# Kernel tuning notes

Hardware: AMD Instinct MI355X
Metric: run time of the kernel (lower is better)

## Reference

```python
import jax, jax.numpy as jnp
import numpy as np

K = 3   # num nearest neighbors (init k)
P = 2   # IDW power (init p)


def setup_inputs() -> dict:
    key = jax.random.key(0)
    k1, k2, k3, k4 = jax.random.split(key, 4)
    B, N, M, C = 8, 16384, 1024, 256
    xyz = jax.random.normal(k1, (B, N, 3), dtype=jnp.float32)
    sampled_xyz = jax.random.normal(k2, (B, M, 3), dtype=jnp.float32)
    sampled_features = jax.random.normal(k3, (B, M, C), dtype=jnp.float32)
    masks = jax.random.randint(k4, (B, N), 0, 2, dtype=jnp.int32)
    return {"xyz": xyz, "sampled_xyz": sampled_xyz,
            "sampled_features": sampled_features, "masks": masks}


def reference(xyz, sampled_xyz, sampled_features, masks):
    # xyz: [B,N,3], sampled_xyz: [B,M,3], sampled_features: [B,M,C], masks: [B,N]
    # Squared pairwise distances [B,N,M] (same math as the chunked torch loop).
    delta = xyz[:, :, None, :] - sampled_xyz[:, None, :, :]
    dists = jnp.sum(delta * delta, axis=-1)
    # k smallest distances -> negate and take top-k.
    neg_top, idx = jax.lax.top_k(-dists, K)          # [B,N,K]
    min_dists = jnp.maximum(-neg_top, 1e-10)
    weights = 1.0 / (min_dists ** P + 1e-10)
    weights = weights / jnp.sum(weights, axis=-1, keepdims=True)
    # Gather neighbor features: [B,N,K,C]
    gathered = jax.vmap(lambda f, i: f[i])(sampled_features, idx)
    interpolated = jnp.sum(gathered * weights[..., None], axis=2)  # [B,N,C]
    # Invalid (masked-out) rows stay zero, matching the padded scatter.
    valid = (masks != 0).astype(interpolated.dtype)
    return interpolated * valid[..., None]
```

## Files before the change

### kernel.cpp

```cpp
#include <hip/hip_runtime.h>

constexpr int B = 8;
constexpr int N = 16384;
constexpr int M = 1024;
constexpr int C = 256;
constexpr int PTS = 128;
constexpr int NW  = 8;
constexpr int CPW = M / NW;

__global__ __launch_bounds__(512, 8) void upsample_idw_kernel(
    const float* __restrict__ xyz,
    const float* __restrict__ sxyz,
    const float* __restrict__ feats,
    const int*   __restrict__ masks,
    float*       __restrict__ out)
{
    const int tid = threadIdx.x;
    const int w   = tid >> 6;
    const int l   = tid & 63;
    const int blk = blockIdx.x;
    const int b     = blk >> 7;
    const int nbase = (blk & 127) << 7;

    __shared__ unsigned long long s_key[PTS][NW][3];
    float4* s_cand = (float4*)&s_key[0][0][0];
    __shared__ float s_w[PTS][3];
    __shared__ int   s_j[PTS][4];

    {
        const float* sp = sxyz + (size_t)b * (M * 3);
        #pragma unroll
        for (int t = tid; t < M; t += 512) {
            const float cx = sp[3 * t + 0];
            const float cy = sp[3 * t + 1];
            const float cz = sp[3 * t + 2];
            s_cand[t] = make_float4(cx, cy, cz, 0.f);
        }
    }

    const float* xpA = xyz + ((size_t)b * N + nbase + l) * 3;
    const float* xpB = xyz + ((size_t)b * N + nbase + l + 64) * 3;
    const float xA = xpA[0], yA = xpA[1], zA = xpA[2];
    const float xB = xpB[0], yB = xpB[1], zB = xpB[2];
    __syncthreads();

    const float4* cp = s_cand + w * CPW;

    float a0 = __builtin_inff(), a1 = __builtin_inff(), a2 = __builtin_inff();
    float b0 = __builtin_inff(), b1 = __builtin_inff(), b2 = __builtin_inff();
    int   ia0 = 0, ia1 = 0, ia2 = 0;
    int   ib0 = 0, ib1 = 0, ib2 = 0;

    #pragma unroll 2
    for (int m = 0; m < CPW; ++m) {
        const float4 c = cp[m];
        {
            const float dx = __fsub_rn(xA, c.x);
            const float dy = __fsub_rn(yA, c.y);
            const float dz = __fsub_rn(zA, c.z);
            const float d  = __fadd_rn(__fadd_rn(__fmul_rn(dx, dx), __fmul_rn(dy, dy)),
                                       __fmul_rn(dz, dz));
            const bool lt0 = d < a0, lt1 = d < a1, lt2 = d < a2;
            ia2 = lt1 ? ia1 : (lt2 ? m : ia2);
            ia1 = lt0 ? ia0 : (lt1 ? m : ia1);
            ia0 = lt0 ? m   : ia0;
            const float nd2 = __builtin_amdgcn_fmed3f(a1, a2, d);
            const float nd1 = __builtin_amdgcn_fmed3f(a0, a1, d);
            a2 = nd2; a1 = nd1; a0 = fminf(a0, d);
        }
        {
            const float dx = __fsub_rn(xB, c.x);
            const float dy = __fsub_rn(yB, c.y);
            const float dz = __fsub_rn(zB, c.z);
            const float d  = __fadd_rn(__fadd_rn(__fmul_rn(dx, dx), __fmul_rn(dy, dy)),
                                       __fmul_rn(dz, dz));
            const bool lt0 = d < b0, lt1 = d < b1, lt2 = d < b2;
            ib2 = lt1 ? ib1 : (lt2 ? m : ib2);
            ib1 = lt0 ? ib0 : (lt1 ? m : ib1);
            ib0 = lt0 ? m   : ib0;
            const float nd2 = __builtin_amdgcn_fmed3f(b1, b2, d);
            const float nd1 = __builtin_amdgcn_fmed3f(b0, b1, d);
            b2 = nd2; b1 = nd1; b0 = fminf(b0, d);
        }
    }
    __syncthreads();

    const unsigned base = (unsigned)(w * CPW);
    s_key[l][w][0]      = ((unsigned long long)__float_as_uint(a0) << 32) | (base + (unsigned)ia0);
    s_key[l][w][1]      = ((unsigned long long)__float_as_uint(a1) << 32) | (base + (unsigned)ia1);
    s_key[l][w][2]      = ((unsigned long long)__float_as_uint(a2) << 32) | (base + (unsigned)ia2);
    s_key[l + 64][w][0] = ((unsigned long long)__float_as_uint(b0) << 32) | (base + (unsigned)ib0);
    s_key[l + 64][w][1] = ((unsigned long long)__float_as_uint(b1) << 32) | (base + (unsigned)ib1);
    s_key[l + 64][w][2] = ((unsigned long long)__float_as_uint(b2) << 32) | (base + (unsigned)ib2);
    __syncthreads();

    if (tid < PTS) {
        unsigned long long k0 = ~0ULL, k1 = ~0ULL, k2 = ~0ULL;
        #pragma unroll
        for (int q = 0; q < NW; ++q) {
            #pragma unroll
            for (int s = 0; s < 3; ++s) {
                const unsigned long long k = s_key[tid][q][s];
                const bool lt0 = k < k0, lt1 = k < k1, lt2 = k < k2;
                k2 = lt1 ? k1 : (lt2 ? k : k2);
                k1 = lt0 ? k0 : (lt1 ? k : k1);
                k0 = lt0 ? k  : k0;
            }
        }
        const float e0 = __uint_as_float((unsigned)(k0 >> 32));
        const float e1 = __uint_as_float((unsigned)(k1 >> 32));
        const float e2 = __uint_as_float((unsigned)(k2 >> 32));
        const float m0 = fmaxf(e0, 1e-10f);
        const float m1 = fmaxf(e1, 1e-10f);
        const float m2 = fmaxf(e2, 1e-10f);
        float w0 = 1.0f / (m0 * m0 + 1e-10f);
        float w1 = 1.0f / (m1 * m1 + 1e-10f);
        float w2 = 1.0f / (m2 * m2 + 1e-10f);
        const int valid = masks[(size_t)b * N + nbase + tid];
        const float scale = valid ? (1.0f / (w0 + w1 + w2)) : 0.0f;
        s_w[tid][0] = w0 * scale;
        s_w[tid][1] = w1 * scale;
        s_w[tid][2] = w2 * scale;
        s_j[tid][0] = (int)(unsigned)k0;
        s_j[tid][1] = (int)(unsigned)k1;
        s_j[tid][2] = (int)(unsigned)k2;
        s_j[tid][3] = valid;
    }
    __syncthreads();

    const int pq = tid >> 6;
    const int cq = tid & 63;
    const float4* Fb4 = (const float4*)(feats + (size_t)b * (M * C));
    float4* op4 = (float4*)(out + (((size_t)b * N + nbase) * C));

    for (int p0 = 0; p0 < PTS; p0 += 8) {
        const int p = p0 + pq;
        const int vld = __builtin_amdgcn_readfirstlane(s_j[p][3]);
        float4 acc = make_float4(0.f, 0.f, 0.f, 0.f);
        if (vld) {
            const int j0 = __builtin_amdgcn_readfirstlane(s_j[p][0]);
            const int j1 = __builtin_amdgcn_readfirstlane(s_j[p][1]);
            const int j2 = __builtin_amdgcn_readfirstlane(s_j[p][2]);
            const float w0 = __uint_as_float(
                __builtin_amdgcn_readfirstlane((int)__float_as_uint(s_w[p][0])));
            const float w1 = __uint_as_float(
                __builtin_amdgcn_readfirstlane((int)__float_as_uint(s_w[p][1])));
            const float w2 = __uint_as_float(
                __builtin_amdgcn_readfirstlane((int)__float_as_uint(s_w[p][2])));
            const float4 f0 = Fb4[j0 * 64 + cq];
            const float4 f1 = Fb4[j1 * 64 + cq];
            const float4 f2 = Fb4[j2 * 64 + cq];
            acc.x = fmaf(w2, f2.x, fmaf(w1, f1.x, w0 * f0.x));
            acc.y = fmaf(w2, f2.y, fmaf(w1, f1.y, w0 * f0.y));
            acc.z = fmaf(w2, f2.z, fmaf(w1, f1.z, w0 * f0.z));
            acc.w = fmaf(w2, f2.w, fmaf(w1, f1.w, w0 * f0.w));
        }
        op4[p * 64 + cq] = acc;
    }
}

extern "C" void kernel_launch(void* const* d_in, const int* in_sizes, int n_in,
                              void* d_out, int out_size, void* d_ws, size_t ws_size,
                              hipStream_t stream) {
    const float* xyz   = (const float*)d_in[0];
    const float* sxyz  = (const float*)d_in[1];
    const float* feats = (const float*)d_in[2];
    const int*   masks = (const int*)d_in[3];
    float*       out   = (float*)d_out;

    dim3 grid(B * N / PTS);
    dim3 block(512);
    hipLaunchKernelGGL(upsample_idw_kernel, grid, block, 0, stream,
                       xyz, sxyz, feats, masks, out);
}
```

Before: 79.93 us.

## Load candidate points via scalar loads into SGPRs instead of LDS staging

Replaces the shared-memory staging of sampled points with inline-asm s_load_dwordx16 scalar loads that bring 16 candidates at a time into SGPRs per wave. This removes the LDS fill, one barrier and the per-iteration LDS reads in the distance loop. The block-to-batch mapping is also interleaved so consecutive blocks hit different batches. The cost is a scalar-memory wait per chunk and reliance on inline asm with the SGPR pressure that brings.

```diff
diff --git a/kernel.cpp b/kernel.cpp
--- a/kernel.cpp
+++ b/kernel.cpp
@@ -6,7 +6,8 @@
 constexpr int C = 256;
 constexpr int PTS = 128;
 constexpr int NW  = 8;
-constexpr int CPW = M / NW;
+
+typedef float vf16 __attribute__((ext_vector_type(16)));
 
 __global__ __launch_bounds__(512, 8) void upsample_idw_kernel(
     const float* __restrict__ xyz,
@@ -19,73 +20,75 @@
     const int w   = tid >> 6;
     const int l   = tid & 63;
     const int blk = blockIdx.x;
-    const int b     = blk >> 7;
-    const int nbase = (blk & 127) << 7;
+    const int b     = blk & 7;
+    const int nbase = (blk >> 3) << 7;
 
     __shared__ unsigned long long s_key[PTS][NW][3];
-    float4* s_cand = (float4*)&s_key[0][0][0];
     __shared__ float s_w[PTS][3];
     __shared__ int   s_j[PTS][4];
 
-    {
-        const float* sp = sxyz + (size_t)b * (M * 3);
-        #pragma unroll
-        for (int t = tid; t < M; t += 512) {
-            const float cx = sp[3 * t + 0];
-            const float cy = sp[3 * t + 1];
-            const float cz = sp[3 * t + 2];
-            s_cand[t] = make_float4(cx, cy, cz, 0.f);
-        }
-    }
-
     const float* xpA = xyz + ((size_t)b * N + nbase + l) * 3;
-    const float* xpB = xyz + ((size_t)b * N + nbase + l + 64) * 3;
+    const float* xpB = xyz + ((size_t)b * N + nbase + 64 + l) * 3;
     const float xA = xpA[0], yA = xpA[1], zA = xpA[2];
     const float xB = xpB[0], yB = xpB[1], zB = xpB[2];
-    __syncthreads();
 
-    const float4* cp = s_cand + w * CPW;
+    const float* bbase = sxyz + (size_t)b * (M * 3);
+    const int qoff = __builtin_amdgcn_readfirstlane((tid >> 6) * (128 * 12));
 
     float a0 = __builtin_inff(), a1 = __builtin_inff(), a2 = __builtin_inff();
     float b0 = __builtin_inff(), b1 = __builtin_inff(), b2 = __builtin_inff();
     int   ia0 = 0, ia1 = 0, ia2 = 0;
     int   ib0 = 0, ib1 = 0, ib2 = 0;
 
-    #pragma unroll 2
-    for (int m = 0; m < CPW; ++m) {
-        const float4 c = cp[m];
-        {
-            const float dx = __fsub_rn(xA, c.x);
-            const float dy = __fsub_rn(yA, c.y);
-            const float dz = __fsub_rn(zA, c.z);
-            const float d  = __fadd_rn(__fadd_rn(__fmul_rn(dx, dx), __fmul_rn(dy, dy)),
-                                       __fmul_rn(dz, dz));
-            const bool lt0 = d < a0, lt1 = d < a1, lt2 = d < a2;
-            ia2 = lt1 ? ia1 : (lt2 ? m : ia2);
-            ia1 = lt0 ? ia0 : (lt1 ? m : ia1);
-            ia0 = lt0 ? m   : ia0;
-            const float nd2 = __builtin_amdgcn_fmed3f(a1, a2, d);
-            const float nd1 = __builtin_amdgcn_fmed3f(a0, a1, d);
-            a2 = nd2; a1 = nd1; a0 = fminf(a0, d);
-        }
-        {
-            const float dx = __fsub_rn(xB, c.x);
-            const float dy = __fsub_rn(yB, c.y);
-            const float dz = __fsub_rn(zB, c.z);
-            const float d  = __fadd_rn(__fadd_rn(__fmul_rn(dx, dx), __fmul_rn(dy, dy)),
-                                       __fmul_rn(dz, dz));
-            const bool lt0 = d < b0, lt1 = d < b1, lt2 = d < b2;
-            ib2 = lt1 ? ib1 : (lt2 ? m : ib2);
-            ib1 = lt0 ? ib0 : (lt1 ? m : ib1);
-            ib0 = lt0 ? m   : ib0;
-            const float nd2 = __builtin_amdgcn_fmed3f(b1, b2, d);
-            const float nd1 = __builtin_amdgcn_fmed3f(b0, b1, d);
-            b2 = nd2; b1 = nd1; b0 = fminf(b0, d);
+    for (int ch = 0; ch < 8; ++ch) {
+        vf16 ca, cb, cc;
+        const int off = qoff + ch * 192;
+        asm volatile(
+            "s_load_dwordx16 %0, %3, %4\n\t"
+            "s_load_dwordx16 %1, %3, %4 offset:64\n\t"
+            "s_load_dwordx16 %2, %3, %4 offset:128\n\t"
+            "s_waitcnt lgkmcnt(0)"
+            : "=&s"(ca), "=&s"(cb), "=&s"(cc)
+            : "s"(bbase), "s"(off));
+        #pragma unroll
+        for (int j = 0; j < 16; ++j) {
+            const int f0 = 3 * j, f1 = 3 * j + 1, f2 = 3 * j + 2;
+            const float cx = (f0 < 16) ? ca[f0 & 15] : (f0 < 32) ? cb[f0 & 15] : cc[f0 & 15];
+            const float cy = (f1 < 16) ? ca[f1 & 15] : (f1 < 32) ? cb[f1 & 15] : cc[f1 & 15];
+            const float cz = (f2 < 16) ? ca[f2 & 15] : (f2 < 32) ? cb[f2 & 15] : cc[f2 & 15];
+            const int m = ch * 16 + j;
+            {
+                const float dx = __fsub_rn(cx, xA);
+                const float dy = __fsub_rn(cy, yA);
+                const float dz = __fsub_rn(cz, zA);
+                const float d  = __fadd_rn(__fadd_rn(__fmul_rn(dx, dx), __fmul_rn(dy, dy)),
+                                           __fmul_rn(dz, dz));
+                const bool lt0 = d < a0, lt1 = d < a1, lt2 = d < a2;
+                ia2 = lt1 ? ia1 : (lt2 ? m : ia2);
+                ia1 = lt0 ? ia0 : (lt1 ? m : ia1);
+                ia0 = lt0 ? m   : ia0;
+                const float nd2 = __builtin_amdgcn_fmed3f(a1, a2, d);
+                const float nd1 = __builtin_amdgcn_fmed3f(a0, a1, d);
+                a2 = nd2; a1 = nd1; a0 = fminf(a0, d);
+            }
+            {
+                const float dx = __fsub_rn(cx, xB);
+                const float dy = __fsub_rn(cy, yB);
+                const float dz = __fsub_rn(cz, zB);
+                const float d  = __fadd_rn(__fadd_rn(__fmul_rn(dx, dx), __fmul_rn(dy, dy)),
+                                           __fmul_rn(dz, dz));
+                const bool lt0 = d < b0, lt1 = d < b1, lt2 = d < b2;
+                ib2 = lt1 ? ib1 : (lt2 ? m : ib2);
+                ib1 = lt0 ? ib0 : (lt1 ? m : ib1);
+                ib0 = lt0 ? m   : ib0;
+                const float nd2 = __builtin_amdgcn_fmed3f(b1, b2, d);
+                const float nd1 = __builtin_amdgcn_fmed3f(b0, b1, d);
+                b2 = nd2; b1 = nd1; b0 = fminf(b0, d);
+            }
         }
     }
-    __syncthreads();
 
-    const unsigned base = (unsigned)(w * CPW);
+    const unsigned base = (unsigned)(w * 128);
     s_key[l][w][0]      = ((unsigned long long)__float_as_uint(a0) << 32) | (base + (unsigned)ia0);
     s_key[l][w][1]      = ((unsigned long long)__float_as_uint(a1) << 32) | (base + (unsigned)ia1);
     s_key[l][w][2]      = ((unsigned long long)__float_as_uint(a2) << 32) | (base + (unsigned)ia2);
@@ -128,13 +131,11 @@
     }
     __syncthreads();
 
-    const int pq = tid >> 6;
-    const int cq = tid & 63;
     const float4* Fb4 = (const float4*)(feats + (size_t)b * (M * C));
     float4* op4 = (float4*)(out + (((size_t)b * N + nbase) * C));
 
-    for (int p0 = 0; p0 < PTS; p0 += 8) {
-        const int p = p0 + pq;
+    for (int i = 0; i < 16; ++i) {
+        const int p = i * 8 + w;
         const int vld = __builtin_amdgcn_readfirstlane(s_j[p][3]);
         float4 acc = make_float4(0.f, 0.f, 0.f, 0.f);
         if (vld) {
@@ -147,15 +148,15 @@
                 __builtin_amdgcn_readfirstlane((int)__float_as_uint(s_w[p][1])));
             const float w2 = __uint_as_float(
                 __builtin_amdgcn_readfirstlane((int)__float_as_uint(s_w[p][2])));
-            const float4 f0 = Fb4[j0 * 64 + cq];
-            const float4 f1 = Fb4[j1 * 64 + cq];
-            const float4 f2 = Fb4[j2 * 64 + cq];
+            const float4 f0 = Fb4[j0 * 64 + l];
+            const float4 f1 = Fb4[j1 * 64 + l];
+            const float4 f2 = Fb4[j2 * 64 + l];
             acc.x = fmaf(w2, f2.x, fmaf(w1, f1.x, w0 * f0.x));
             acc.y = fmaf(w2, f2.y, fmaf(w1, f1.y, w0 * f0.y));
             acc.z = fmaf(w2, f2.z, fmaf(w1, f1.z, w0 * f0.z));
             acc.w = fmaf(w2, f2.w, fmaf(w1, f1.w, w0 * f0.w));
         }
-        op4[p * 64 + cq] = acc;
+        op4[p * 64 + l] = acc;
     }
 }
 
```

Result: slower. 101.6 us (+27.0%).
